# Kernel tuning notes

Hardware: AMD Instinct MI355X
Metric: run time of the kernel (lower is better)

## Reference

```python
import jax, jax.numpy as jnp
import numpy as np

N_QUBITS = 4
Q_DEPTH = 6
Q_DELTA = 0.01
INPUT_SIZE = 64
BATCH = 262144


def _ry_gate(theta):
    # RY(theta) = [[cos(t/2), -sin(t/2)], [sin(t/2), cos(t/2)]]; theta scalar or (B,)
    c = jnp.cos(theta / 2)
    s = jnp.sin(theta / 2)
    return jnp.stack([jnp.stack([c, -s], -1), jnp.stack([s, c], -1)], -2)


def _apply_1q(state, gate, wire):
    # state: (B,2,2,2,2); gate: (2,2) shared or (B,2,2) per-sample
    ax = wire + 1
    s = jnp.moveaxis(state, ax, -1)
    if gate.ndim == 2:
        s = jnp.einsum('ij,b...j->b...i', gate, s)
    else:
        s = jnp.einsum('bij,b...j->b...i', gate, s)
    return jnp.moveaxis(s, -1, ax)


def _apply_cnot(state, ctrl, tgt):
    ca, ta = ctrl + 1, tgt + 1
    s0 = jnp.take(state, jnp.array([0]), axis=ca)
    s1 = jnp.take(state, jnp.array([1]), axis=ca)
    s1 = jnp.flip(s1, axis=ta)  # X on target where control=1
    return jnp.concatenate([s0, s1], axis=ca)


def _quantum_net(q_in, q_weights):
    # q_in: (B, 4) per-sample RY angles; q_weights: (Q_DEPTH, 4)
    B = q_in.shape[0]
    # H layer on |0000>: uniform real amplitude 1/4 over all 16 basis states
    state = jnp.full((B,) + (2,) * N_QUBITS, 0.25, dtype=q_in.dtype)
    for w in range(N_QUBITS):
        state = _apply_1q(state, _ry_gate(q_in[:, w]), w)
    for k in range(Q_DEPTH):
        for i in range(0, N_QUBITS - 1, 2):
            state = _apply_cnot(state, i, i + 1)
        for i in range(1, N_QUBITS - 1, 2):
            state = _apply_cnot(state, i, i + 1)
        for w in range(N_QUBITS):
            state = _apply_1q(state, _ry_gate(q_weights[k, w]), w)
    # All gates are real -> real statevector; probs = amp^2
    probs = state * state
    signs = jnp.array([1.0, -1.0], dtype=state.dtype)
    expz = []
    for w in range(N_QUBITS):
        shp = [1] * (N_QUBITS + 1)
        shp[w + 1] = 2
        expz.append(jnp.sum(probs * signs.reshape(shp), axis=tuple(range(1, N_QUBITS + 1))))
    return jnp.stack(expz, axis=-1)  # (B, 4)


def setup_inputs() -> dict:
    key = jax.random.key(0)
    k1, k2, k3, k4, k5, k6 = jax.random.split(key, 6)
    bound_pre = 1.0 / np.sqrt(INPUT_SIZE)
    bound_post = 1.0 / np.sqrt(N_QUBITS)
    return {
        'input_features': jax.random.normal(k1, (BATCH, INPUT_SIZE), dtype=jnp.float32),
        'pre_w': jax.random.uniform(k2, (N_QUBITS, INPUT_SIZE), jnp.float32, -bound_pre, bound_pre),
        'pre_b': jax.random.uniform(k3, (N_QUBITS,), jnp.float32, -bound_pre, bound_pre),
        'q_params': Q_DELTA * jax.random.normal(k4, (Q_DEPTH * N_QUBITS,), dtype=jnp.float32),
        'post_w': jax.random.uniform(k5, (1, N_QUBITS), jnp.float32, -bound_post, bound_post),
        'post_b': jax.random.uniform(k6, (1,), jnp.float32, -bound_post, bound_post),
    }


def reference(input_features, pre_w, pre_b, q_params, post_w, post_b):
    pre_out = input_features @ pre_w.T + pre_b
    q_in = jnp.tanh(pre_out) * (jnp.pi / 2.0)
    q_out = _quantum_net(q_in, q_params.reshape(Q_DEPTH, N_QUBITS))
    return q_out @ post_w.T + post_b  # (B, 1)
```

## Files before the change

### kernel.cpp

```cpp
#include <hip/hip_runtime.h>
#include <math.h>

#define NQ      4
#define QDEPTH  6
#define TPB     256
#define ROWLEN  64

__device__ __forceinline__ float fast_tanh(float x) {
    float e = __expf(2.0f * x);
    float r = __builtin_amdgcn_rcpf(e + 1.0f);
    return fmaf(-2.0f, r, 1.0f);
}

template<int W>
__device__ __forceinline__ void apply_ry(float st[16], float c, float s) {
    constexpr int M = 8 >> W;
#pragma unroll
    for (int i = 0; i < 16; ++i) {
        if ((i & M) == 0) {
            float a0 = st[i];
            float a1 = st[i | M];
            st[i]     = fmaf(c, a0, -(s * a1));
            st[i | M] = fmaf(s, a0,  (c * a1));
        }
    }
}

template<int C, int T>
__device__ __forceinline__ void apply_cnot(float st[16]) {
    constexpr int MC = 8 >> C;
    constexpr int MT = 8 >> T;
#pragma unroll
    for (int i = 0; i < 16; ++i) {
        if ((i & MC) != 0 && (i & MT) == 0) {
            float tmp = st[i];
            st[i] = st[i | MT];
            st[i | MT] = tmp;
        }
    }
}

__global__ __launch_bounds__(TPB, 4) void dqnet_kernel(
    const float* __restrict__ inp,
    const float* __restrict__ pre_w,
    const float* __restrict__ pre_b,
    const float* __restrict__ qp,
    const float* __restrict__ post_w,
    const float* __restrict__ post_b,
    float* __restrict__ out)
{
    __shared__ float4 tile[4 * 512];
    __shared__ float cw[QDEPTH * NQ];
    __shared__ float sw[QDEPTH * NQ];
    __shared__ float gg[16];

    const int t = threadIdx.x;

    if (t < QDEPTH * NQ) {
        float h = 0.5f * qp[t];
        cw[t] = __cosf(h);
        sw[t] = __sinf(h);
    } else if (t >= 32 && t < 48) {
        int i = t - 32;
        float v = 0.0f;
#pragma unroll
        for (int w = 0; w < NQ; ++w) {
            float p = post_w[w];
            v += ((i >> (3 - w)) & 1) ? -p : p;
        }
        gg[i] = v;
    }
    __syncthreads();

    const int wave = t >> 6;
    const int lane = t & 63;
    const size_t wrow0 = (size_t)blockIdx.x * TPB + wave * 64;
    const float4* gp = (const float4*)(inp + wrow0 * ROWLEN);
    float4* wt = &tile[wave * 512];
    const float4* pw4 = (const float4*)pre_w;

    float4 x0[8], x1[8];
#pragma unroll
    for (int j = 0; j < 8; ++j) {
        int idx = j * 64 + lane;
        int rw = idx >> 3, c = idx & 7;
        x0[j] = gp[rw * 16 + c];
    }
#pragma unroll
    for (int j = 0; j < 8; ++j) {
        int idx = j * 64 + lane;
        int rw = idx >> 3, c = idx & 7;
        wt[rw * 8 + (c ^ (rw & 7))] = x0[j];
    }
#pragma unroll
    for (int j = 0; j < 8; ++j) {
        int idx = j * 64 + lane;
        int rw = idx >> 3, c = idx & 7;
        x1[j] = gp[rw * 16 + 8 + c];
    }

    float acc0 = pre_b[0], acc1 = pre_b[1], acc2 = pre_b[2], acc3 = pre_b[3];
#pragma unroll
    for (int i = 0; i < 8; ++i) {
        float4 x  = wt[lane * 8 + (i ^ (lane & 7))];
        float4 w0 = pw4[0 * 16 + i];
        float4 w1 = pw4[1 * 16 + i];
        float4 w2 = pw4[2 * 16 + i];
        float4 w3 = pw4[3 * 16 + i];
        acc0 = fmaf(x.x, w0.x, acc0); acc0 = fmaf(x.y, w0.y, acc0);
        acc0 = fmaf(x.z, w0.z, acc0); acc0 = fmaf(x.w, w0.w, acc0);
        acc1 = fmaf(x.x, w1.x, acc1); acc1 = fmaf(x.y, w1.y, acc1);
        acc1 = fmaf(x.z, w1.z, acc1); acc1 = fmaf(x.w, w1.w, acc1);
        acc2 = fmaf(x.x, w2.x, acc2); acc2 = fmaf(x.y, w2.y, acc2);
        acc2 = fmaf(x.z, w2.z, acc2); acc2 = fmaf(x.w, w2.w, acc2);
        acc3 = fmaf(x.x, w3.x, acc3); acc3 = fmaf(x.y, w3.y, acc3);
        acc3 = fmaf(x.z, w3.z, acc3); acc3 = fmaf(x.w, w3.w, acc3);
    }

#pragma unroll
    for (int j = 0; j < 8; ++j) {
        int idx = j * 64 + lane;
        int rw = idx >> 3, c = idx & 7;
        wt[rw * 8 + (c ^ (rw & 7))] = x1[j];
    }
#pragma unroll
    for (int i = 0; i < 8; ++i) {
        float4 x  = wt[lane * 8 + (i ^ (lane & 7))];
        float4 w0 = pw4[0 * 16 + 8 + i];
        float4 w1 = pw4[1 * 16 + 8 + i];
        float4 w2 = pw4[2 * 16 + 8 + i];
        float4 w3 = pw4[3 * 16 + 8 + i];
        acc0 = fmaf(x.x, w0.x, acc0); acc0 = fmaf(x.y, w0.y, acc0);
        acc0 = fmaf(x.z, w0.z, acc0); acc0 = fmaf(x.w, w0.w, acc0);
        acc1 = fmaf(x.x, w1.x, acc1); acc1 = fmaf(x.y, w1.y, acc1);
        acc1 = fmaf(x.z, w1.z, acc1); acc1 = fmaf(x.w, w1.w, acc1);
        acc2 = fmaf(x.x, w2.x, acc2); acc2 = fmaf(x.y, w2.y, acc2);
        acc2 = fmaf(x.z, w2.z, acc2); acc2 = fmaf(x.w, w2.w, acc2);
        acc3 = fmaf(x.x, w3.x, acc3); acc3 = fmaf(x.y, w3.y, acc3);
        acc3 = fmaf(x.z, w3.z, acc3); acc3 = fmaf(x.w, w3.w, acc3);
    }

    const float QK = 0.78539816339744831f;
    float h0 = fast_tanh(acc0) * QK;
    float h1 = fast_tanh(acc1) * QK;
    float h2 = fast_tanh(acc2) * QK;
    float h3 = fast_tanh(acc3) * QK;
    float c0 = __cosf(h0), s0 = __sinf(h0);
    float c1 = __cosf(h1), s1 = __sinf(h1);
    float c2 = __cosf(h2), s2 = __sinf(h2);
    float c3 = __cosf(h3), s3 = __sinf(h3);

    const float R = 0.70710678118654752f;
    float u0 = (c0 - s0) * R, v0 = (c0 + s0) * R;
    float u1 = (c1 - s1) * R, v1 = (c1 + s1) * R;
    float u2 = (c2 - s2) * R, v2 = (c2 + s2) * R;
    float u3 = (c3 - s3) * R, v3 = (c3 + s3) * R;

    float p00 = u0 * u1, p01 = u0 * v1, p10 = v0 * u1, p11 = v0 * v1;
    float q00 = u2 * u3, q01 = u2 * v3, q10 = v2 * u3, q11 = v2 * v3;

    float st[16];
    st[ 0] = p00 * q00; st[ 1] = p00 * q01; st[ 2] = p00 * q10; st[ 3] = p00 * q11;
    st[ 4] = p01 * q00; st[ 5] = p01 * q01; st[ 6] = p01 * q10; st[ 7] = p01 * q11;
    st[ 8] = p10 * q00; st[ 9] = p10 * q01; st[10] = p10 * q10; st[11] = p10 * q11;
    st[12] = p11 * q00; st[13] = p11 * q01; st[14] = p11 * q10; st[15] = p11 * q11;

#pragma unroll
    for (int k = 0; k < QDEPTH; ++k) {
        apply_cnot<0, 1>(st);
        apply_cnot<2, 3>(st);
        apply_cnot<1, 2>(st);
        apply_ry<0>(st, cw[k * 4 + 0], sw[k * 4 + 0]);
        apply_ry<1>(st, cw[k * 4 + 1], sw[k * 4 + 1]);
        apply_ry<2>(st, cw[k * 4 + 2], sw[k * 4 + 2]);
        apply_ry<3>(st, cw[k * 4 + 3], sw[k * 4 + 3]);
    }

    float r = post_b[0];
#pragma unroll
    for (int i = 0; i < 16; ++i)
        r = fmaf(st[i] * st[i], gg[i], r);

    out[wrow0 + lane] = r;
}

extern "C" void kernel_launch(void* const* d_in, const int* in_sizes, int n_in,
                              void* d_out, int out_size, void* d_ws, size_t ws_size,
                              hipStream_t stream) {
    const float* inp    = (const float*)d_in[0];
    const float* pre_w  = (const float*)d_in[1];
    const float* pre_b  = (const float*)d_in[2];
    const float* qp     = (const float*)d_in[3];
    const float* post_w = (const float*)d_in[4];
    const float* post_b = (const float*)d_in[5];
    float* out = (float*)d_out;

    int n = in_sizes[0] / ROWLEN;
    int grid = n / TPB;
    dqnet_kernel<<<grid, TPB, 0, stream>>>(inp, pre_w, pre_b, qp, post_w, post_b, out);
}
```

Before: 101.9 us.

## Precompute circuit observable as trig polynomial coefficients and evaluate per sample

Each block now builds the fixed circuit unitary and the observable matrix M = U^T diag(g) U in shared memory. It reduces M into an 81-coefficient trigonometric tensor in the per-sample angles, so each row costs only a small polynomial in sin/cos instead of 6 layers of 16-amplitude gate simulation. The goal is to remove most per-sample ALU work from the statevector loop. The cost is a chain of block-level barriers and redundant per-block setup, though this is partly overlapped with the second half of the input load, which now happens earlier.

```diff
diff --git a/kernel.cpp b/kernel.cpp
--- a/kernel.cpp
+++ b/kernel.cpp
@@ -10,6 +10,11 @@
     float e = __expf(2.0f * x);
     float r = __builtin_amdgcn_rcpf(e + 1.0f);
     return fmaf(-2.0f, r, 1.0f);
+}
+
+__device__ __forceinline__ void lds_fence_barrier() {
+    asm volatile("s_waitcnt lgkmcnt(0)" ::: "memory");
+    __builtin_amdgcn_s_barrier();
 }
 
 template<int W>
@@ -50,28 +55,13 @@
     float* __restrict__ out)
 {
     __shared__ float4 tile[4 * 512];
-    __shared__ float cw[QDEPTH * NQ];
-    __shared__ float sw[QDEPTH * NQ];
-    __shared__ float gg[16];
+    __shared__ float cs[QDEPTH * NQ], sn[QDEPTH * NQ], gg[16];
+    __shared__ float Ush[16][16];
+    __shared__ float Msh[16][16];
+    __shared__ float S1[192], S2[144], S3[108];
+    __shared__ float Tsh[81];
 
     const int t = threadIdx.x;
-
-    if (t < QDEPTH * NQ) {
-        float h = 0.5f * qp[t];
-        cw[t] = __cosf(h);
-        sw[t] = __sinf(h);
-    } else if (t >= 32 && t < 48) {
-        int i = t - 32;
-        float v = 0.0f;
-#pragma unroll
-        for (int w = 0; w < NQ; ++w) {
-            float p = post_w[w];
-            v += ((i >> (3 - w)) & 1) ? -p : p;
-        }
-        gg[i] = v;
-    }
-    __syncthreads();
-
     const int wave = t >> 6;
     const int lane = t & 63;
     const size_t wrow0 = (size_t)blockIdx.x * TPB + wave * 64;
@@ -90,13 +80,109 @@
     for (int j = 0; j < 8; ++j) {
         int idx = j * 64 + lane;
         int rw = idx >> 3, c = idx & 7;
+        x1[j] = gp[rw * 16 + 8 + c];
+    }
+
+    if (t < QDEPTH * NQ) {
+        float h = 0.5f * qp[t];
+        cs[t] = __cosf(h);
+        sn[t] = __sinf(h);
+    } else if (t >= 32 && t < 48) {
+        int i = t - 32;
+        float v = 0.0f;
+#pragma unroll
+        for (int w = 0; w < NQ; ++w) {
+            float p = post_w[w];
+            v += ((i >> (3 - w)) & 1) ? -p : p;
+        }
+        gg[i] = v;
+    }
+    lds_fence_barrier();
+
+    if (t < 16) {
+        float st[16];
+#pragma unroll
+        for (int i = 0; i < 16; ++i) st[i] = (i == t) ? 1.0f : 0.0f;
+#pragma unroll
+        for (int k = 0; k < QDEPTH; ++k) {
+            apply_cnot<0, 1>(st);
+            apply_cnot<2, 3>(st);
+            apply_cnot<1, 2>(st);
+            apply_ry<0>(st, cs[k * 4 + 0], sn[k * 4 + 0]);
+            apply_ry<1>(st, cs[k * 4 + 1], sn[k * 4 + 1]);
+            apply_ry<2>(st, cs[k * 4 + 2], sn[k * 4 + 2]);
+            apply_ry<3>(st, cs[k * 4 + 3], sn[k * 4 + 3]);
+        }
+#pragma unroll
+        for (int k = 0; k < 16; ++k) Ush[k][t] = st[k];
+    }
+    lds_fence_barrier();
+
+    {
+        int i = t >> 4, j = t & 15;
+        float m = 0.0f;
+#pragma unroll
+        for (int k = 0; k < 16; ++k)
+            m = fmaf(gg[k] * Ush[k][i], Ush[k][j], m);
+        Msh[i][j] = m;
+    }
+    lds_fence_barrier();
+
+    if (t < 192) {
+        int e0 = t >> 6, r = t & 63;
+        int p1 = r >> 4, p2 = (r >> 2) & 3, p3 = r & 3;
+        auto Rv = [&](int p0) {
+            int i = ((p0 >> 1) << 3) | ((p1 >> 1) << 2) | ((p2 >> 1) << 1) | (p3 >> 1);
+            int j = ((p0 & 1) << 3) | ((p1 & 1) << 2) | ((p2 & 1) << 1) | (p3 & 1);
+            return Msh[i][j];
+        };
+        float v = (e0 == 0) ? 0.5f * (Rv(0) + Rv(3))
+                : (e0 == 1) ? 0.5f * (Rv(3) - Rv(0))
+                            : 0.5f * (Rv(1) + Rv(2));
+        S1[e0 * 64 + r] = v;
+    }
+    lds_fence_barrier();
+
+    if (t < 144) {
+        int e0 = t / 48, rem = t % 48;
+        int e1 = rem >> 4, r2 = rem & 15;
+        const float* base = &S1[e0 * 64];
+        auto g1 = [&](int p1) { return base[p1 * 16 + r2]; };
+        float v = (e1 == 0) ? 0.5f * (g1(0) + g1(3))
+                : (e1 == 1) ? 0.5f * (g1(3) - g1(0))
+                            : 0.5f * (g1(1) + g1(2));
+        S2[(e0 * 3 + e1) * 16 + r2] = v;
+    }
+    lds_fence_barrier();
+
+    if (t < 108) {
+        int e01 = t / 12, rem = t % 12;
+        int e2 = rem >> 2, p3 = rem & 3;
+        const float* base = &S2[e01 * 16];
+        auto g2 = [&](int p2) { return base[p2 * 4 + p3]; };
+        float v = (e2 == 0) ? 0.5f * (g2(0) + g2(3))
+                : (e2 == 1) ? 0.5f * (g2(3) - g2(0))
+                            : 0.5f * (g2(1) + g2(2));
+        S3[(e01 * 3 + e2) * 4 + p3] = v;
+    }
+    lds_fence_barrier();
+
+    if (t < 81) {
+        int e012 = t / 3, e3 = t % 3;
+        const float* base = &S3[e012 * 4];
+        float v = (e3 == 0) ? 0.5f * (base[0] + base[3])
+                : (e3 == 1) ? 0.5f * (base[3] - base[0])
+                            : 0.5f * (base[1] + base[2]);
+        if (t == 0) v += post_b[0];
+        Tsh[t] = v;
+    }
+    lds_fence_barrier();
+
+#pragma unroll
+    for (int j = 0; j < 8; ++j) {
+        int idx = j * 64 + lane;
+        int rw = idx >> 3, c = idx & 7;
         wt[rw * 8 + (c ^ (rw & 7))] = x0[j];
-    }
-#pragma unroll
-    for (int j = 0; j < 8; ++j) {
-        int idx = j * 64 + lane;
-        int rw = idx >> 3, c = idx & 7;
-        x1[j] = gp[rw * 16 + 8 + c];
     }
 
     float acc0 = pre_b[0], acc1 = pre_b[1], acc2 = pre_b[2], acc3 = pre_b[3];
@@ -140,46 +226,33 @@
         acc3 = fmaf(x.z, w3.z, acc3); acc3 = fmaf(x.w, w3.w, acc3);
     }
 
-    const float QK = 0.78539816339744831f;
-    float h0 = fast_tanh(acc0) * QK;
-    float h1 = fast_tanh(acc1) * QK;
-    float h2 = fast_tanh(acc2) * QK;
-    float h3 = fast_tanh(acc3) * QK;
-    float c0 = __cosf(h0), s0 = __sinf(h0);
-    float c1 = __cosf(h1), s1 = __sinf(h1);
-    float c2 = __cosf(h2), s2 = __sinf(h2);
-    float c3 = __cosf(h3), s3 = __sinf(h3);
-
-    const float R = 0.70710678118654752f;
-    float u0 = (c0 - s0) * R, v0 = (c0 + s0) * R;
-    float u1 = (c1 - s1) * R, v1 = (c1 + s1) * R;
-    float u2 = (c2 - s2) * R, v2 = (c2 + s2) * R;
-    float u3 = (c3 - s3) * R, v3 = (c3 + s3) * R;
-
-    float p00 = u0 * u1, p01 = u0 * v1, p10 = v0 * u1, p11 = v0 * v1;
-    float q00 = u2 * u3, q01 = u2 * v3, q10 = v2 * u3, q11 = v2 * v3;
-
-    float st[16];
-    st[ 0] = p00 * q00; st[ 1] = p00 * q01; st[ 2] = p00 * q10; st[ 3] = p00 * q11;
-    st[ 4] = p01 * q00; st[ 5] = p01 * q01; st[ 6] = p01 * q10; st[ 7] = p01 * q11;
-    st[ 8] = p10 * q00; st[ 9] = p10 * q01; st[10] = p10 * q10; st[11] = p10 * q11;
-    st[12] = p11 * q00; st[13] = p11 * q01; st[14] = p11 * q10; st[15] = p11 * q11;
-
-#pragma unroll
-    for (int k = 0; k < QDEPTH; ++k) {
-        apply_cnot<0, 1>(st);
-        apply_cnot<2, 3>(st);
-        apply_cnot<1, 2>(st);
-        apply_ry<0>(st, cw[k * 4 + 0], sw[k * 4 + 0]);
-        apply_ry<1>(st, cw[k * 4 + 1], sw[k * 4 + 1]);
-        apply_ry<2>(st, cw[k * 4 + 2], sw[k * 4 + 2]);
-        apply_ry<3>(st, cw[k * 4 + 3], sw[k * 4 + 3]);
-    }
-
-    float r = post_b[0];
-#pragma unroll
-    for (int i = 0; i < 16; ++i)
-        r = fmaf(st[i] * st[i], gg[i], r);
+    const float QH = 1.57079632679489662f;
+    float th0 = fast_tanh(acc0) * QH;
+    float th1 = fast_tanh(acc1) * QH;
+    float th2 = fast_tanh(acc2) * QH;
+    float th3 = fast_tanh(acc3) * QH;
+    float s0 = __sinf(th0), c0 = __cosf(th0);
+    float s1 = __sinf(th1), c1 = __cosf(th1);
+    float s2 = __sinf(th2), c2 = __cosf(th2);
+    float s3 = __sinf(th3), c3 = __cosf(th3);
+
+    float r = 0.0f;
+#pragma unroll
+    for (int e0 = 0; e0 < 3; ++e0) {
+        float a0 = 0.0f;
+#pragma unroll
+        for (int e1 = 0; e1 < 3; ++e1) {
+            float a1 = 0.0f;
+#pragma unroll
+            for (int e2 = 0; e2 < 3; ++e2) {
+                const float* tb = &Tsh[((e0 * 3 + e1) * 3 + e2) * 3];
+                float w = fmaf(c3, tb[2], fmaf(s3, tb[1], tb[0]));
+                a1 = (e2 == 0) ? (a1 + w) : (e2 == 1) ? fmaf(s2, w, a1) : fmaf(c2, w, a1);
+            }
+            a0 = (e1 == 0) ? (a0 + a1) : (e1 == 1) ? fmaf(s1, a1, a0) : fmaf(c1, a1, a0);
+        }
+        r = (e0 == 0) ? (r + a0) : (e0 == 1) ? fmaf(s0, a0, r) : fmaf(c0, a0, r);
+    }
 
     out[wrow0 + lane] = r;
 }
```

New measurement: 126.1 us. 1.24x slower.
